# Kernel optimization log

Measured on AMD Instinct MI355X. Metric: run time of the kernel, lower is better.

## Reference

```python
import jax, jax.numpy as jnp
import numpy as np

TOP_K = 2
NUM_EXPERTS = 8

def setup_inputs() -> dict:
    key = jax.random.key(0)
    k_x, k_r, k_g, k_u, k_d = jax.random.split(key, 5)
    B, L, D, H, E = 1, 2048, 1024, 2048, NUM_EXPERTS
    scale = 0.02  # keep router logits / activations in a sane range
    return {
        "x": jax.random.normal(k_x, (B, L, D), dtype=jnp.float32),
        "router_w": jax.random.normal(k_r, (D, E), dtype=jnp.float32) * scale,
        "gate_w": jax.random.normal(k_g, (E, D, H), dtype=jnp.float32) * scale,
        "up_w": jax.random.normal(k_u, (E, D, H), dtype=jnp.float32) * scale,
        "down_w": jax.random.normal(k_d, (E, H, D), dtype=jnp.float32) * scale,
    }

def reference(x, router_w, gate_w, up_w, down_w):
    # x: (B, L, D)
    B, L, D = x.shape
    T = B * L
    E = router_w.shape[1]
    xf = x.reshape(T, D)

    # --- router: top-k softmax over selected logits (Mixtral-style) ---
    logits = xf @ router_w                      # (T, E)
    top_vals, top_idx = jax.lax.top_k(logits, TOP_K)  # (T, K)
    top_w = jax.nn.softmax(top_vals, axis=-1)   # (T, K)

    # combine weights scattered to dense (T, E); zeros for unrouted experts
    combine = jnp.zeros((T, E), dtype=x.dtype).at[
        jnp.arange(T)[:, None], top_idx
    ].add(top_w)

    # --- experts: SwiGLU, computed per expert, zero-weight tokens masked by combine ---
    gate = jnp.einsum('td,edh->eth', xf, gate_w)   # (E, T, H)
    up = jnp.einsum('td,edh->eth', xf, up_w)       # (E, T, H)
    hidden = jax.nn.silu(gate) * up                # (E, T, H)
    expert_out = jnp.einsum('eth,ehd->etd', hidden, down_w)  # (E, T, D)

    # --- weighted combine (equivalent to scatter_add over sorted assignments) ---
    y = jnp.einsum('etd,te->td', expert_out, combine)  # (T, D)
    return y.reshape(B, L, D)
```

## Files before the change

### kernel.cpp

```cpp
#include <hip/hip_runtime.h>
#include <hip/hip_bf16.h>
#include <stdint.h>

#define T_TOK 2048
#define DIM   1024
#define HDIM  2048
#define NE    8
#define ROWS_PAD 4224
#define TSLOTS 40

typedef __attribute__((ext_vector_type(8))) short bf16x8;
typedef __attribute__((ext_vector_type(8))) unsigned short u16x8;
typedef __attribute__((ext_vector_type(4))) float f32x4;

__device__ __forceinline__ unsigned short f2bf(float f) {
    union { float f; unsigned int u; } v; v.f = f;
    unsigned int r = v.u + 0x7FFF + ((v.u >> 16) & 1);
    return (unsigned short)(r >> 16);
}

__device__ __forceinline__ float bf2f(unsigned short b) {
    union { unsigned int u; float f; } v; v.u = ((unsigned int)b) << 16;
    return v.f;
}

__device__ __forceinline__ void gload16(const void* g, void* l) {
    __builtin_amdgcn_global_load_lds(
        (const __attribute__((address_space(1))) void*)g,
        (__attribute__((address_space(3))) void*)l, 16, 0, 0);
}

__global__ void router_kernel(const float* __restrict__ x, const float* __restrict__ rw,
                              int* __restrict__ counts, int* __restrict__ top_idx,
                              float* __restrict__ top_w) {
    int wid = (blockIdx.x * blockDim.x + threadIdx.x) >> 6;
    int lane = threadIdx.x & 63;
    if (wid >= T_TOK) return;
    float acc[NE];
#pragma unroll
    for (int e = 0; e < NE; ++e) acc[e] = 0.f;
    const float* xr = x + (size_t)wid * DIM;
    for (int i = lane; i < DIM; i += 64) {
        float xv = xr[i];
        const float* wr = rw + (size_t)i * NE;
#pragma unroll
        for (int e = 0; e < NE; ++e) acc[e] += xv * wr[e];
    }
#pragma unroll
    for (int off = 32; off; off >>= 1) {
#pragma unroll
        for (int e = 0; e < NE; ++e) acc[e] += __shfl_xor(acc[e], off, 64);
    }
    if (lane == 0) {
        float v0 = -1e30f, v1 = -1e30f; int i0 = 0, i1 = 0;
#pragma unroll
        for (int e = 0; e < NE; ++e) {
            float v = acc[e];
            if (v > v0) { v1 = v0; i1 = i0; v0 = v; i0 = e; }
            else if (v > v1) { v1 = v; i1 = e; }
        }
        float e1 = __expf(v1 - v0);
        float s = 1.f + e1;
        top_idx[wid * 2]     = i0;
        top_idx[wid * 2 + 1] = i1;
        top_w[wid * 2]     = 1.f / s;
        top_w[wid * 2 + 1] = e1 / s;
        atomicAdd(&counts[i0], 1);
        atomicAdd(&counts[i1], 1);
    }
}

__global__ void scan_kernel(const int* __restrict__ counts, int* __restrict__ offsets,
                            int* __restrict__ cursors,
                            int* __restrict__ tl_e, int* __restrict__ tl_m) {
    if (threadIdx.x == 0) {
        int run = 0;
        for (int e = 0; e < NE; ++e) { offsets[e] = run; cursors[e] = run; run += counts[e]; }
        int n = 0;
        for (int e = 0; e < NE; ++e) {
            int mt = (counts[e] + 127) >> 7;
            for (int m = 0; m < mt && n < 64; ++m) { tl_e[n] = e; tl_m[n] = m; ++n; }
        }
        for (; n < 64; ++n) tl_e[n] = -1;
    }
}

__global__ void gather_kernel(const float* __restrict__ x, const int* __restrict__ top_idx,
                              const float* __restrict__ top_w, int* __restrict__ cursors,
                              int* __restrict__ row_tok, float* __restrict__ row_w,
                              unsigned short* __restrict__ Abuf) {
    int t = blockIdx.x;
    __shared__ int pos[2];
    if (threadIdx.x < 2) {
        int k = threadIdx.x;
        int e = top_idx[t * 2 + k];
        int p = atomicAdd(&cursors[e], 1);
        pos[k] = p;
        row_tok[p] = t;
        row_w[p] = top_w[t * 2 + k];
    }
    __syncthreads();
    const float4* xr = (const float4*)(x + (size_t)t * DIM);
    float4 v = xr[threadIdx.x];
    ushort4 b;
    b.x = f2bf(v.x); b.y = f2bf(v.y); b.z = f2bf(v.z); b.w = f2bf(v.w);
    ushort4* A4 = (ushort4*)Abuf;
    A4[(size_t)pos[0] * (DIM / 4) + threadIdx.x] = b;
    A4[(size_t)pos[1] * (DIM / 4) + threadIdx.x] = b;
}

__global__ __launch_bounds__(256, 2)
void gemm1_kernel(const unsigned short* __restrict__ Abuf,
                  const float* __restrict__ gw,
                  const float* __restrict__ uw,
                  unsigned short* __restrict__ Hbuf,
                  const int* __restrict__ offsets, const int* __restrict__ counts,
                  const int* __restrict__ tl_e, const int* __restrict__ tl_m) {
    const int slot = blockIdx.y;
    const int e = tl_e[slot];
    if (e < 0) return;
    const int mtile = tl_m[slot];
    const int cnt = counts[e];
    const int n0 = blockIdx.x * 64;
    const int row0 = offsets[e] + mtile * 128;

    __shared__ __align__(16) unsigned char lds_raw[65536];
    unsigned short* AsB = (unsigned short*)lds_raw;
    unsigned short* BgB = (unsigned short*)(lds_raw + 32768);
    unsigned short* BuB = (unsigned short*)(lds_raw + 49152);
    unsigned short* ex  = (unsigned short*)lds_raw;

    const int tid = threadIdx.x;
    const int lane = tid & 63;
    const int wave = tid >> 6;
    const int wm = wave >> 1;
    const int wu = wave & 1;

    f32x4 acc[4][4];
#pragma unroll
    for (int i = 0; i < 4; ++i)
#pragma unroll
        for (int j = 0; j < 4; ++j) acc[i][j] = (f32x4){0.f, 0.f, 0.f, 0.f};

    const int srow = tid >> 3;
    const int sc0 = tid & 7;
    const unsigned short* Aab = Abuf + (size_t)row0 * DIM;

    auto stageA = [&](int buf, int kt) {
#pragma unroll
        for (int i = 0; i < 4; ++i) {
            int row = i * 32 + srow;
            int csrc = sc0 ^ (row & 7);
            gload16(Aab + (size_t)row * DIM + kt + csrc * 8,
                    AsB + buf * 8192 + (i * 256 + tid) * 8);
        }
    };

    const int bn = tid & 63;
    const int bc0 = tid >> 6;
    const float* Bgb = gw + (size_t)e * DIM * HDIM + n0 + bn;
    const float* Bub = uw + (size_t)e * DIM * HDIM + n0 + bn;

    float bgl[2][8], bul[2][8];
    auto bload = [&](int kt) {
#pragma unroll
        for (int cc = 0; cc < 2; ++cc) {
            int c = bc0 + cc * 4;
            const float* gs = Bgb + (size_t)(kt + c * 8) * HDIM;
            const float* us = Bub + (size_t)(kt + c * 8) * HDIM;
#pragma unroll
            for (int jj = 0; jj < 8; ++jj) {
                bgl[cc][jj] = gs[(size_t)jj * HDIM];
                bul[cc][jj] = us[(size_t)jj * HDIM];
            }
        }
    };
    auto bwrite = [&](int buf) {
#pragma unroll
        for (int cc = 0; cc < 2; ++cc) {
            int c = bc0 + cc * 4;
            int la = bn * 64 + ((c ^ (bn & 7)) * 8);
            u16x8 vg, vu;
#pragma unroll
            for (int jj = 0; jj < 8; ++jj) {
                vg[jj] = f2bf(bgl[cc][jj]);
                vu[jj] = f2bf(bul[cc][jj]);
            }
            *(u16x8*)&BgB[buf * 4096 + la] = vg;
            *(u16x8*)&BuB[buf * 4096 + la] = vu;
        }
    };

    const int rsel = lane & 15;
    const int csrcf = lane >> 4;

    stageA(0, 0);
    bload(0);
    bwrite(0);
    int cur = 0;
    for (int kt = 0; kt < DIM; kt += 64) {
        __syncthreads();
        const bool pre = (kt + 64 < DIM);
        if (pre) { stageA(cur ^ 1, kt + 64); bload(kt + 64); }
        const unsigned short* Ac = AsB + cur * 8192;
        const unsigned short* Bc = (wu ? BuB : BgB) + cur * 4096;
#pragma unroll
        for (int kk = 0; kk < 2; ++kk) {
            bf16x8 af[4], bb[4];
#pragma unroll
            for (int i = 0; i < 4; ++i) {
                int ra = wm * 64 + i * 16 + rsel;
                af[i] = *(const bf16x8*)&Ac[ra * 64 + ((kk * 4 + csrcf) ^ (ra & 7)) * 8];
                int rb = i * 16 + rsel;
                bb[i] = *(const bf16x8*)&Bc[rb * 64 + ((kk * 4 + csrcf) ^ (rb & 7)) * 8];
            }
#pragma unroll
            for (int i = 0; i < 4; ++i)
#pragma unroll
                for (int j = 0; j < 4; ++j)
                    acc[i][j] = __builtin_amdgcn_mfma_f32_16x16x32_bf16(af[i], bb[j], acc[i][j], 0, 0, 0);
        }
        if (pre) bwrite(cur ^ 1);
        cur ^= 1;
    }

    const int c = lane & 15, rbase = (lane >> 4) * 4;
    const int obase = offsets[e];
    __syncthreads();
    if (wu) {
#pragma unroll
        for (int i = 0; i < 4; ++i)
#pragma unroll
            for (int r = 0; r < 4; ++r) {
                int row64 = i * 16 + rbase + r;
#pragma unroll
                for (int j = 0; j < 4; ++j)
                    ex[wm * 4096 + row64 * 64 + j * 16 + c] = f2bf(acc[i][j][r]);
            }
    }
    __syncthreads();
    if (!wu) {
#pragma unroll
        for (int i = 0; i < 4; ++i) {
#pragma unroll
            for (int r = 0; r < 4; ++r) {
                int row64 = i * 16 + rbase + r;
                int lrow = mtile * 128 + wm * 64 + row64;
                if (lrow < cnt) {
                    size_t orow = (size_t)(obase + lrow);
#pragma unroll
                    for (int j = 0; j < 4; ++j) {
                        float g = acc[i][j][r];
                        float u = bf2f(ex[wm * 4096 + row64 * 64 + j * 16 + c]);
                        float h = g * u / (1.f + __expf(-g));
                        Hbuf[orow * HDIM + n0 + j * 16 + c] = f2bf(h);
                    }
                }
            }
        }
    }
}

__global__ __launch_bounds__(256, 2)
void gemm2_kernel(const unsigned short* __restrict__ Hbuf,
                  const float* __restrict__ dw,
                  float* __restrict__ y,
                  const int* __restrict__ offsets, const int* __restrict__ counts,
                  const int* __restrict__ row_tok, const float* __restrict__ row_w,
                  const int* __restrict__ tl_e, const int* __restrict__ tl_m) {
    const int slot = blockIdx.y;
    const int e = tl_e[slot];
    if (e < 0) return;
    const int mtile = tl_m[slot];
    const int kc = blockIdx.z;
    const int cnt = counts[e];
    const int n0 = blockIdx.x * 128;
    const int row0 = offsets[e] + mtile * 128;

    __shared__ unsigned short As[2][128 * 64];
    __shared__ unsigned short Bs[2][128 * 64];

    const int tid = threadIdx.x;
    const int lane = tid & 63;
    const int wave = tid >> 6;
    const int wm = wave >> 1, wn = wave & 1;

    f32x4 acc[4][4];
#pragma unroll
    for (int i = 0; i < 4; ++i)
#pragma unroll
        for (int j = 0; j < 4; ++j) acc[i][j] = (f32x4){0.f, 0.f, 0.f, 0.f};

    const int srow0 = tid >> 3;
    const int sc0 = tid & 7;
    const unsigned short* Aab = Hbuf + (size_t)row0 * HDIM;

    auto stageA = [&](int buf, int kt) {
#pragma unroll
        for (int i = 0; i < 4; ++i) {
            int row = i * 32 + srow0;
            int csrc = sc0 ^ (row & 7);
            gload16(Aab + (size_t)row * HDIM + kt + csrc * 8,
                    &As[buf][(i * 256 + tid) * 8]);
        }
    };

    const int bn = tid & 127;
    const int bc0 = (tid >> 7) * 4;
    const float* Bbb = dw + (size_t)e * HDIM * DIM + n0 + bn;

    float bl[4][8];
    auto bload = [&](int kt) {
#pragma unroll
        for (int cc = 0; cc < 4; ++cc) {
            const float* bs = Bbb + (size_t)(kt + (bc0 + cc) * 8) * DIM;
#pragma unroll
            for (int jj = 0; jj < 8; ++jj)
                bl[cc][jj] = bs[(size_t)jj * DIM];
        }
    };
    auto bwrite = [&](int buf) {
#pragma unroll
        for (int cc = 0; cc < 4; ++cc) {
            int c = bc0 + cc;
            int la = bn * 64 + ((c ^ (bn & 7)) * 8);
            u16x8 v;
#pragma unroll
            for (int jj = 0; jj < 8; ++jj) v[jj] = f2bf(bl[cc][jj]);
            *(u16x8*)&Bs[buf][la] = v;
        }
    };

    const int rsel = lane & 15;
    const int csrcf = lane >> 4;

    const int kbeg = kc * (HDIM / 2);
    const int kend = kbeg + (HDIM / 2);

    stageA(0, kbeg);
    bload(kbeg);
    bwrite(0);
    int cur = 0;
    for (int kt = kbeg; kt < kend; kt += 64) {
        __syncthreads();
        const bool pre = (kt + 64 < kend);
        if (pre) { stageA(cur ^ 1, kt + 64); bload(kt + 64); }
        const unsigned short* Ac = As[cur];
        const unsigned short* Bc = Bs[cur];
#pragma unroll
        for (int kk = 0; kk < 2; ++kk) {
            bf16x8 af[4], bf[4];
#pragma unroll
            for (int i = 0; i < 4; ++i) {
                int ra = wm * 64 + i * 16 + rsel;
                af[i] = *(const bf16x8*)&Ac[ra * 64 + ((kk * 4 + csrcf) ^ (ra & 7)) * 8];
                int rb = wn * 64 + i * 16 + rsel;
                bf[i] = *(const bf16x8*)&Bc[rb * 64 + ((kk * 4 + csrcf) ^ (rb & 7)) * 8];
            }
#pragma unroll
            for (int i = 0; i < 4; ++i)
#pragma unroll
                for (int j = 0; j < 4; ++j)
                    acc[i][j] = __builtin_amdgcn_mfma_f32_16x16x32_bf16(af[i], bf[j], acc[i][j], 0, 0, 0);
        }
        if (pre) bwrite(cur ^ 1);
        cur ^= 1;
    }

    const int c = lane & 15, rbase = (lane >> 4) * 4;
    const int obase = offsets[e];
#pragma unroll
    for (int i = 0; i < 4; ++i) {
#pragma unroll
        for (int r = 0; r < 4; ++r) {
            int lrow = mtile * 128 + wm * 64 + i * 16 + rbase + r;
            if (lrow < cnt) {
                int grow = obase + lrow;
                int tok = row_tok[grow];
                float w = row_w[grow];
#pragma unroll
                for (int j = 0; j < 4; ++j) {
                    atomicAdd(&y[(size_t)tok * DIM + n0 + wn * 64 + j * 16 + c], w * acc[i][j][r]);
                }
            }
        }
    }
}

extern "C" void kernel_launch(void* const* d_in, const int* in_sizes, int n_in,
                              void* d_out, int out_size, void* d_ws, size_t ws_size,
                              hipStream_t stream) {
    const float* x  = (const float*)d_in[0];
    const float* rw = (const float*)d_in[1];
    const float* gw = (const float*)d_in[2];
    const float* uw = (const float*)d_in[3];
    const float* dw = (const float*)d_in[4];
    float* y = (float*)d_out;

    char* ws = (char*)d_ws;
    int*   counts  = (int*)(ws + 0);
    int*   cursors = (int*)(ws + 32);
    int*   offsets = (int*)(ws + 64);
    int*   top_idx = (int*)(ws + 128);
    float* top_w   = (float*)(ws + 128 + 16384);
    int*   row_tok = (int*)(ws + 128 + 32768);
    float* row_w   = (float*)(ws + 128 + 32768 + 16896);
    int*   tl_e    = (int*)(ws + 128 + 32768 + 2 * 16896);
    int*   tl_m    = (int*)(ws + 128 + 32768 + 2 * 16896 + 256);
    size_t off = 128 + 32768 + 2 * 16896 + 512;
    off = (off + 255) & ~(size_t)255;
    unsigned short* Abuf = (unsigned short*)(ws + off); off += (size_t)ROWS_PAD * DIM * 2;
    unsigned short* Hbuf = (unsigned short*)(ws + off); off += (size_t)ROWS_PAD * HDIM * 2;
    if (ws_size < off) return;

    hipMemsetAsync(counts, 0, 32, stream);
    hipMemsetAsync(d_out, 0, (size_t)out_size * 4, stream);

    router_kernel<<<T_TOK / 4, 256, 0, stream>>>(x, rw, counts, top_idx, top_w);
    scan_kernel<<<1, 64, 0, stream>>>(counts, offsets, cursors, tl_e, tl_m);
    gather_kernel<<<T_TOK, 256, 0, stream>>>(x, top_idx, top_w, cursors, row_tok, row_w, Abuf);

    gemm1_kernel<<<dim3(HDIM / 64, TSLOTS), 256, 0, stream>>>(Abuf, gw, uw, Hbuf,
                                                              offsets, counts, tl_e, tl_m);
    gemm2_kernel<<<dim3(DIM / 128, TSLOTS, 2), 256, 0, stream>>>(Hbuf, dw, y, offsets, counts,
                                                                 row_tok, row_w, tl_e, tl_m);
}
```

Baseline: 249.1 us.

## Stage GEMM tiles through registers with two-deep prefetch and single barriers

Both expert GEMM kernels stop using global_load_lds for the A tiles and instead load A and B tiles into two register sets. The loop is unrolled by two so tile k+2 is fetched while tile k is computed, and tile k+1 is written to LDS. Each stage is fenced by one lgkmcnt wait plus a raw s_barrier instead of __syncthreads. The aim is to hide more global load latency behind the MFMA work. The cost is many extra VGPRs for the doubled staging buffers, which may lower occupancy, and A data now makes an extra trip through registers.

```diff
diff --git a/kernel.cpp b/kernel.cpp
--- a/kernel.cpp
+++ b/kernel.cpp
@@ -22,12 +22,6 @@
 __device__ __forceinline__ float bf2f(unsigned short b) {
     union { unsigned int u; float f; } v; v.u = ((unsigned int)b) << 16;
     return v.f;
-}
-
-__device__ __forceinline__ void gload16(const void* g, void* l) {
-    __builtin_amdgcn_global_load_lds(
-        (const __attribute__((address_space(1))) void*)g,
-        (__attribute__((address_space(3))) void*)l, 16, 0, 0);
 }
 
 __global__ void router_kernel(const float* __restrict__ x, const float* __restrict__ rw,
@@ -146,82 +140,87 @@
     const int sc0 = tid & 7;
     const unsigned short* Aab = Abuf + (size_t)row0 * DIM;
 
-    auto stageA = [&](int buf, int kt) {
-#pragma unroll
-        for (int i = 0; i < 4; ++i) {
-            int row = i * 32 + srow;
-            int csrc = sc0 ^ (row & 7);
-            gload16(Aab + (size_t)row * DIM + kt + csrc * 8,
-                    AsB + buf * 8192 + (i * 256 + tid) * 8);
-        }
-    };
-
     const int bn = tid & 63;
     const int bc0 = tid >> 6;
     const float* Bgb = gw + (size_t)e * DIM * HDIM + n0 + bn;
     const float* Bub = uw + (size_t)e * DIM * HDIM + n0 + bn;
 
-    float bgl[2][8], bul[2][8];
-    auto bload = [&](int kt) {
-#pragma unroll
-        for (int cc = 0; cc < 2; ++cc) {
-            int c = bc0 + cc * 4;
-            const float* gs = Bgb + (size_t)(kt + c * 8) * HDIM;
-            const float* us = Bub + (size_t)(kt + c * 8) * HDIM;
-#pragma unroll
-            for (int jj = 0; jj < 8; ++jj) {
-                bgl[cc][jj] = gs[(size_t)jj * HDIM];
-                bul[cc][jj] = us[(size_t)jj * HDIM];
-            }
-        }
-    };
-    auto bwrite = [&](int buf) {
-#pragma unroll
-        for (int cc = 0; cc < 2; ++cc) {
-            int c = bc0 + cc * 4;
-            int la = bn * 64 + ((c ^ (bn & 7)) * 8);
-            u16x8 vg, vu;
-#pragma unroll
-            for (int jj = 0; jj < 8; ++jj) {
-                vg[jj] = f2bf(bgl[cc][jj]);
-                vu[jj] = f2bf(bul[cc][jj]);
-            }
-            *(u16x8*)&BgB[buf * 4096 + la] = vg;
-            *(u16x8*)&BuB[buf * 4096 + la] = vu;
-        }
-    };
+    u16x8 aT0[4], aT1[4];
+    float bg0[2][8], bu0[2][8], bg1[2][8], bu1[2][8];
+
+#define G1_ALOAD(aT, kt) do {                                              \
+    _Pragma("unroll") for (int i = 0; i < 4; ++i) {                        \
+        int row_ = i * 32 + srow;                                          \
+        int csrc_ = sc0 ^ (row_ & 7);                                      \
+        aT[i] = *(const u16x8*)&Aab[(size_t)row_ * DIM + (kt) + csrc_ * 8];\
+    } } while (0)
+
+#define G1_AWRITE(aT, buf) do {                                            \
+    _Pragma("unroll") for (int i = 0; i < 4; ++i)                          \
+        *(u16x8*)&AsB[(buf) * 8192 + (i * 256 + tid) * 8] = aT[i];         \
+    } while (0)
+
+#define G1_BLOAD(bg, bu, kt) do {                                          \
+    _Pragma("unroll") for (int cc = 0; cc < 2; ++cc) {                     \
+        int c_ = bc0 + cc * 4;                                             \
+        const float* gs_ = Bgb + (size_t)((kt) + c_ * 8) * HDIM;           \
+        const float* us_ = Bub + (size_t)((kt) + c_ * 8) * HDIM;           \
+        _Pragma("unroll") for (int jj = 0; jj < 8; ++jj) {                 \
+            bg[cc][jj] = gs_[(size_t)jj * HDIM];                           \
+            bu[cc][jj] = us_[(size_t)jj * HDIM];                           \
+        } } } while (0)
+
+#define G1_BWRITE(bg, bu, buf) do {                                        \
+    _Pragma("unroll") for (int cc = 0; cc < 2; ++cc) {                     \
+        int c_ = bc0 + cc * 4;                                             \
+        int la_ = bn * 64 + ((c_ ^ (bn & 7)) * 8);                         \
+        u16x8 vg_, vu_;                                                    \
+        _Pragma("unroll") for (int jj = 0; jj < 8; ++jj) {                 \
+            vg_[jj] = f2bf(bg[cc][jj]);                                    \
+            vu_[jj] = f2bf(bu[cc][jj]);                                    \
+        }                                                                  \
+        *(u16x8*)&BgB[(buf) * 4096 + la_] = vg_;                           \
+        *(u16x8*)&BuB[(buf) * 4096 + la_] = vu_;                           \
+    } } while (0)
 
     const int rsel = lane & 15;
     const int csrcf = lane >> 4;
 
-    stageA(0, 0);
-    bload(0);
-    bwrite(0);
-    int cur = 0;
-    for (int kt = 0; kt < DIM; kt += 64) {
-        __syncthreads();
-        const bool pre = (kt + 64 < DIM);
-        if (pre) { stageA(cur ^ 1, kt + 64); bload(kt + 64); }
-        const unsigned short* Ac = AsB + cur * 8192;
-        const unsigned short* Bc = (wu ? BuB : BgB) + cur * 4096;
-#pragma unroll
-        for (int kk = 0; kk < 2; ++kk) {
-            bf16x8 af[4], bb[4];
-#pragma unroll
-            for (int i = 0; i < 4; ++i) {
-                int ra = wm * 64 + i * 16 + rsel;
-                af[i] = *(const bf16x8*)&Ac[ra * 64 + ((kk * 4 + csrcf) ^ (ra & 7)) * 8];
-                int rb = i * 16 + rsel;
-                bb[i] = *(const bf16x8*)&Bc[rb * 64 + ((kk * 4 + csrcf) ^ (rb & 7)) * 8];
-            }
-#pragma unroll
-            for (int i = 0; i < 4; ++i)
-#pragma unroll
-                for (int j = 0; j < 4; ++j)
-                    acc[i][j] = __builtin_amdgcn_mfma_f32_16x16x32_bf16(af[i], bb[j], acc[i][j], 0, 0, 0);
-        }
-        if (pre) bwrite(cur ^ 1);
-        cur ^= 1;
+#define G1_COMPUTE(buf) do {                                               \
+    const unsigned short* Ac_ = AsB + (buf) * 8192;                        \
+    const unsigned short* Bc_ = (wu ? BuB : BgB) + (buf) * 4096;           \
+    _Pragma("unroll") for (int kk = 0; kk < 2; ++kk) {                     \
+        bf16x8 af_[4], bb_[4];                                             \
+        _Pragma("unroll") for (int i = 0; i < 4; ++i) {                    \
+            int ra_ = wm * 64 + i * 16 + rsel;                             \
+            af_[i] = *(const bf16x8*)&Ac_[ra_ * 64 + ((kk * 4 + csrcf) ^ (ra_ & 7)) * 8]; \
+            int rb_ = i * 16 + rsel;                                       \
+            bb_[i] = *(const bf16x8*)&Bc_[rb_ * 64 + ((kk * 4 + csrcf) ^ (rb_ & 7)) * 8]; \
+        }                                                                  \
+        _Pragma("unroll") for (int i = 0; i < 4; ++i)                      \
+            _Pragma("unroll") for (int j = 0; j < 4; ++j)                  \
+                acc[i][j] = __builtin_amdgcn_mfma_f32_16x16x32_bf16(af_[i], bb_[j], acc[i][j], 0, 0, 0); \
+    } } while (0)
+
+#define G1_BAR() do {                                                      \
+    asm volatile("s_waitcnt lgkmcnt(0)" ::: "memory");                     \
+    __builtin_amdgcn_s_barrier();                                          \
+    } while (0)
+
+    G1_ALOAD(aT0, 0);   G1_BLOAD(bg0, bu0, 0);
+    G1_ALOAD(aT1, 64);  G1_BLOAD(bg1, bu1, 64);
+    G1_AWRITE(aT0, 0);  G1_BWRITE(bg0, bu0, 0);
+    G1_BAR();
+
+    for (int k = 0; k < 16; k += 2) {
+        if (k + 2 < 16) { G1_ALOAD(aT0, (k + 2) * 64); G1_BLOAD(bg0, bu0, (k + 2) * 64); }
+        G1_COMPUTE(0);
+        G1_AWRITE(aT1, 1); G1_BWRITE(bg1, bu1, 1);
+        G1_BAR();
+        if (k + 3 < 16) { G1_ALOAD(aT1, (k + 3) * 64); G1_BLOAD(bg1, bu1, (k + 3) * 64); }
+        G1_COMPUTE(1);
+        if (k + 2 < 16) { G1_AWRITE(aT0, 0); G1_BWRITE(bg0, bu0, 0); }
+        G1_BAR();
     }
 
     const int c = lane & 15, rbase = (lane >> 4) * 4;
@@ -291,80 +290,85 @@
 #pragma unroll
         for (int j = 0; j < 4; ++j) acc[i][j] = (f32x4){0.f, 0.f, 0.f, 0.f};
 
-    const int srow0 = tid >> 3;
+    const int srow = tid >> 3;
     const int sc0 = tid & 7;
     const unsigned short* Aab = Hbuf + (size_t)row0 * HDIM;
-
-    auto stageA = [&](int buf, int kt) {
-#pragma unroll
-        for (int i = 0; i < 4; ++i) {
-            int row = i * 32 + srow0;
-            int csrc = sc0 ^ (row & 7);
-            gload16(Aab + (size_t)row * HDIM + kt + csrc * 8,
-                    &As[buf][(i * 256 + tid) * 8]);
-        }
-    };
 
     const int bn = tid & 127;
     const int bc0 = (tid >> 7) * 4;
     const float* Bbb = dw + (size_t)e * HDIM * DIM + n0 + bn;
 
-    float bl[4][8];
-    auto bload = [&](int kt) {
-#pragma unroll
-        for (int cc = 0; cc < 4; ++cc) {
-            const float* bs = Bbb + (size_t)(kt + (bc0 + cc) * 8) * DIM;
-#pragma unroll
-            for (int jj = 0; jj < 8; ++jj)
-                bl[cc][jj] = bs[(size_t)jj * DIM];
-        }
-    };
-    auto bwrite = [&](int buf) {
-#pragma unroll
-        for (int cc = 0; cc < 4; ++cc) {
-            int c = bc0 + cc;
-            int la = bn * 64 + ((c ^ (bn & 7)) * 8);
-            u16x8 v;
-#pragma unroll
-            for (int jj = 0; jj < 8; ++jj) v[jj] = f2bf(bl[cc][jj]);
-            *(u16x8*)&Bs[buf][la] = v;
-        }
-    };
+    u16x8 aT0[4], aT1[4];
+    float bl0[4][8], bl1[4][8];
+
+#define G2_ALOAD(aT, kt) do {                                              \
+    _Pragma("unroll") for (int i = 0; i < 4; ++i) {                        \
+        int row_ = i * 32 + srow;                                          \
+        int csrc_ = sc0 ^ (row_ & 7);                                      \
+        aT[i] = *(const u16x8*)&Aab[(size_t)row_ * HDIM + (kt) + csrc_ * 8]; \
+    } } while (0)
+
+#define G2_AWRITE(aT, buf) do {                                            \
+    _Pragma("unroll") for (int i = 0; i < 4; ++i)                          \
+        *(u16x8*)&As[buf][(i * 256 + tid) * 8] = aT[i];                    \
+    } while (0)
+
+#define G2_BLOAD(bl, kt) do {                                              \
+    _Pragma("unroll") for (int cc = 0; cc < 4; ++cc) {                     \
+        const float* bs_ = Bbb + (size_t)((kt) + (bc0 + cc) * 8) * DIM;    \
+        _Pragma("unroll") for (int jj = 0; jj < 8; ++jj)                   \
+            bl[cc][jj] = bs_[(size_t)jj * DIM];                            \
+    } } while (0)
+
+#define G2_BWRITE(bl, buf) do {                                            \
+    _Pragma("unroll") for (int cc = 0; cc < 4; ++cc) {                     \
+        int c_ = bc0 + cc;                                                 \
+        int la_ = bn * 64 + ((c_ ^ (bn & 7)) * 8);                         \
+        u16x8 v_;                                                          \
+        _Pragma("unroll") for (int jj = 0; jj < 8; ++jj) v_[jj] = f2bf(bl[cc][jj]); \
+        *(u16x8*)&Bs[buf][la_] = v_;                                       \
+    } } while (0)
 
     const int rsel = lane & 15;
     const int csrcf = lane >> 4;
 
+#define G2_COMPUTE(buf) do {                                               \
+    const unsigned short* Ac_ = As[buf];                                   \
+    const unsigned short* Bc_ = Bs[buf];                                   \
+    _Pragma("unroll") for (int kk = 0; kk < 2; ++kk) {                     \
+        bf16x8 af_[4], bf_[4];                                             \
+        _Pragma("unroll") for (int i = 0; i < 4; ++i) {                    \
+            int ra_ = wm * 64 + i * 16 + rsel;                             \
+            af_[i] = *(const bf16x8*)&Ac_[ra_ * 64 + ((kk * 4 + csrcf) ^ (ra_ & 7)) * 8]; \
+            int rb_ = wn * 64 + i * 16 + rsel;                             \
+            bf_[i] = *(const bf16x8*)&Bc_[rb_ * 64 + ((kk * 4 + csrcf) ^ (rb_ & 7)) * 8]; \
+        }                                                                  \
+        _Pragma("unroll") for (int i = 0; i < 4; ++i)                      \
+            _Pragma("unroll") for (int j = 0; j < 4; ++j)                  \
+                acc[i][j] = __builtin_amdgcn_mfma_f32_16x16x32_bf16(af_[i], bf_[j], acc[i][j], 0, 0, 0); \
+    } } while (0)
+
+#define G2_BAR() do {                                                      \
+    asm volatile("s_waitcnt lgkmcnt(0)" ::: "memory");                     \
+    __builtin_amdgcn_s_barrier();                                          \
+    } while (0)
+
     const int kbeg = kc * (HDIM / 2);
-    const int kend = kbeg + (HDIM / 2);
-
-    stageA(0, kbeg);
-    bload(kbeg);
-    bwrite(0);
-    int cur = 0;
-    for (int kt = kbeg; kt < kend; kt += 64) {
-        __syncthreads();
-        const bool pre = (kt + 64 < kend);
-        if (pre) { stageA(cur ^ 1, kt + 64); bload(kt + 64); }
-        const unsigned short* Ac = As[cur];
-        const unsigned short* Bc = Bs[cur];
-#pragma unroll
-        for (int kk = 0; kk < 2; ++kk) {
-            bf16x8 af[4], bf[4];
-#pragma unroll
-            for (int i = 0; i < 4; ++i) {
-                int ra = wm * 64 + i * 16 + rsel;
-                af[i] = *(const bf16x8*)&Ac[ra * 64 + ((kk * 4 + csrcf) ^ (ra & 7)) * 8];
-                int rb = wn * 64 + i * 16 + rsel;
-                bf[i] = *(const bf16x8*)&Bc[rb * 64 + ((kk * 4 + csrcf) ^ (rb & 7)) * 8];
-            }
-#pragma unroll
-            for (int i = 0; i < 4; ++i)
-#pragma unroll
-                for (int j = 0; j < 4; ++j)
-                    acc[i][j] = __builtin_amdgcn_mfma_f32_16x16x32_bf16(af[i], bf[j], acc[i][j], 0, 0, 0);
-        }
-        if (pre) bwrite(cur ^ 1);
-        cur ^= 1;
+
+    G2_ALOAD(aT0, kbeg);      G2_BLOAD(bl0, kbeg);
+    G2_ALOAD(aT1, kbeg + 64); G2_BLOAD(bl1, kbeg + 64);
+    G2_AWRITE(aT0, 0);        G2_BWRITE(bl0, 0);
+    G2_BAR();
+
+    for (int k = 0; k < 16; k += 2) {
+        if (k + 2 < 16) { G2_ALOAD(aT0, kbeg + (k + 2) * 64); G2_BLOAD(bl0, kbeg + (k + 2) * 64); }
+        G2_COMPUTE(0);
+        G2_AWRITE(aT1, 1); G2_BWRITE(bl1, 1);
+        G2_BAR();
+        if (k + 3 < 16) { G2_ALOAD(aT1, kbeg + (k + 3) * 64); G2_BLOAD(bl1, kbeg + (k + 3) * 64); }
+        G2_COMPUTE(1);
+        if (k + 2 < 16) { G2_AWRITE(aT0, 0); G2_BWRITE(bl0, 0); }
+        G2_BAR();
     }
 
     const int c = lane & 15, rbase = (lane >> 4) * 4;
```

Result: slower. 263.6 us (+5.8%).
